# Performance work log

Measured on AMD Instinct MI355X. Metric: run time of the kernel, lower is better.

The kernel has to match this reference:

```python
import jax, jax.numpy as jnp
import numpy as np
from jax.scipy.linalg import expm

D_DYN = 512
STATIC_DIM = 64
U_DIM = 32
N_OBS = 20 * 2 + 10  # num_prod*2 + num_inj
BATCH = 512
T_STEPS = 256


def setup_inputs() -> dict:
    key = jax.random.key(0)
    ks = jax.random.split(key, 9)
    d = D_DYN
    return {
        "z_dyn": jax.random.normal(ks[0], (BATCH, d), jnp.float32),
        "z_static": jax.random.normal(ks[1], (BATCH, STATIC_DIM), jnp.float32),
        "dt": jax.random.uniform(ks[2], (1, 1), jnp.float32),
        "U": jax.random.normal(ks[3], (T_STEPS, BATCH, U_DIM), jnp.float32),
        "A_skew_params": (jax.random.normal(ks[4], (d * (d - 1) // 2,), jnp.float32) * 0.01),
        "gamma_raw": jnp.ones((d,), jnp.float32) * 0.5,
        "B_ct": jax.random.normal(ks[5], (d, U_DIM), jnp.float32) * (1.0 / np.sqrt(U_DIM)),
        "C": jax.random.normal(ks[6], (N_OBS, d), jnp.float32) * (1.0 / np.sqrt(d)),
        "D": jax.random.normal(ks[7], (N_OBS, U_DIM), jnp.float32) * (1.0 / np.sqrt(U_DIM)),
    }


def reference(z_dyn, z_static, dt, U, A_skew_params, gamma_raw, B_ct, C, D):
    d = z_dyn.shape[1]
    # Build continuous-time generator: skew-symmetric part minus positive diagonal damping.
    iu = jnp.triu_indices(d, k=1)
    A_skew = jnp.zeros((d, d), A_skew_params.dtype).at[iu].set(A_skew_params)
    A_skew = A_skew - A_skew.T
    A_ct = A_skew - jnp.diag(jax.nn.softplus(gamma_raw))
    # Exact ZOH discretization: A_bar = expm(A*dt), B_bar = A^{-1}(A_bar - I) B
    dt_val = dt[0, 0]
    A_bar = expm(A_ct * dt_val)
    B_bar = jnp.linalg.solve(A_ct, (A_bar - jnp.eye(d, dtype=A_ct.dtype)) @ B_ct)
    A_bar_T, B_bar_T, C_T, D_T = A_bar.T, B_bar.T, C.T, D.T

    def step(z, ut):
        z = z @ A_bar_T + ut @ B_bar_T          # [B, d]
        y = z @ C_T + (ut * dt) @ D_T           # [B, n_obs]
        return z, (z, y)

    _, (Z, Y) = jax.lax.scan(step, z_dyn, U)    # Z: [T, B, d], Y: [T, B, n_obs]
    return Z, Y
```

## Files before the change

### kernel.cpp

```cpp
#include <hip/hip_runtime.h>
#include <stdint.h>


typedef __bf16 bf16x8 __attribute__((ext_vector_type(8)));
typedef float  f32x4  __attribute__((ext_vector_type(4)));

#define NE  576
#define NE3 1728

__device__ __forceinline__ unsigned short f2bf(float x){
  union { float f; unsigned int u; } v; v.f = x;
  unsigned int r = (v.u + 0x7fffu + ((v.u >> 16) & 1u)) >> 16;
  return (unsigned short)r;
}
__device__ __forceinline__ float bf2f(unsigned short h){
  union { float f; unsigned int u; } v; v.u = ((unsigned int)h) << 16;
  return v.f;
}

__device__ __forceinline__ void gll16(const void* g, void* l){
  __builtin_amdgcn_global_load_lds((__attribute__((address_space(1))) void*)g,
                                   (__attribute__((address_space(3))) void*)l,
                                   16, 0, 0);
}

__global__ __launch_bounds__(256) void k_build_M(
    const float* __restrict__ skew, const float* __restrict__ gamma,
    const float* __restrict__ dtp, const float* __restrict__ B_ct,
    float* __restrict__ Xf, unsigned short* __restrict__ XAp,
    unsigned short* __restrict__ XBt){
  int id = blockIdx.x * 256 + threadIdx.x;
  if (id >= NE * NE) return;
  int r = id / NE, c = id % NE;
  float sc = dtp[0] * 0.25f;
  float v = 0.f;
  if (r < 512 && c < 512) {
    if (r < c) {
      long k = 511L * r - (long)r * (r - 1) / 2 + (c - r - 1);
      v = skew[k];
    } else if (r > c) {
      long k = 511L * c - (long)c * (c - 1) / 2 + (r - c - 1);
      v = -skew[k];
    } else {
      float g = gamma[r];
      float sp = (g > 20.f) ? g : log1pf(expf(g));
      v = -sp;
    }
  } else if (r < 512 && c >= 512 && c < 544) {
    v = B_ct[r * 32 + (c - 512)];
  }
  v *= sc;
  Xf[id] = v;
  unsigned short hi = f2bf(v);
  unsigned short lo = f2bf(v - bf2f(hi));
  XAp[(long)r * NE3 + c]          = hi;
  XAp[(long)r * NE3 + NE + c]     = hi;
  XAp[(long)r * NE3 + 2 * NE + c] = lo;
  XBt[(long)c * NE3 + r]          = hi;
  XBt[(long)c * NE3 + NE + r]     = lo;
  XBt[(long)c * NE3 + 2 * NE + r] = hi;
}

__global__ __launch_bounds__(256) void k_expm_gemm(
    const unsigned short* __restrict__ Ap, const unsigned short* __restrict__ Bt,
    const float* __restrict__ Cadd, float* __restrict__ outF,
    unsigned short* __restrict__ outAp, unsigned short* __restrict__ outBt){
  __shared__ __align__(16) unsigned short As[2][32 * 192];
  __shared__ __align__(16) unsigned short Bs[2][32 * 192];
  int tid = threadIdx.x, wave = tid >> 6, lane = tid & 63;
  int wm = wave & 1, wn = wave >> 1;
  int m0 = blockIdx.y * 32, n0 = blockIdx.x * 32;
  int lr = lane & 15, kq = lane >> 4;
  f32x4 acc = {0.f, 0.f, 0.f, 0.f};
  auto stage = [&](int buf, int kt){
    #pragma unroll
    for (int i = 0; i < 3; i++) {
      int base = i * 256 + wave * 64;
      int cc = base + lane;
      int rr = cc / 24, sl = cc - rr * 24;
      int ss = (sl & 24) | ((sl & 7) ^ (rr & 7));
      gll16(Ap + (long)(m0 + rr) * NE3 + kt + ss * 8, &As[buf][base * 8]);
      gll16(Bt + (long)(n0 + rr) * NE3 + kt + ss * 8, &Bs[buf][base * 8]);
    }
  };
  stage(0, 0);
  int cur = 0;
  for (int kt = 0; kt < NE3; kt += 192) {
    if (kt + 192 < NE3) {
      stage(cur ^ 1, kt + 192);
      asm volatile("s_waitcnt vmcnt(6)" ::: "memory");
    } else {
      asm volatile("s_waitcnt vmcnt(0)" ::: "memory");
    }
    __builtin_amdgcn_s_barrier();
    __builtin_amdgcn_sched_barrier(0);
    #pragma unroll
    for (int hh = 0; hh < 6; hh++) {
      int eo = (hh * 32 + kq * 8) ^ ((lr & 7) << 3);
      bf16x8 af = *(const bf16x8*)&As[cur][(wm * 16 + lr) * 192 + eo];
      bf16x8 bf = *(const bf16x8*)&Bs[cur][(wn * 16 + lr) * 192 + eo];
      acc = __builtin_amdgcn_mfma_f32_16x16x32_bf16(af, bf, acc, 0, 0, 0);
    }
    __builtin_amdgcn_s_barrier();
    cur ^= 1;
  }
  int n = n0 + wn * 16 + lr;
  for (int i = 0; i < 4; i++) {
    int m = m0 + wm * 16 + kq * 4 + i;
    float v = acc[i];
    if (Cadd) v += Cadd[(long)m * NE + n];
    if (outF) outF[(long)m * NE + n] = v;
    unsigned short hi = f2bf(v);
    unsigned short lo = f2bf(v - bf2f(hi));
    if (outAp) {
      outAp[(long)m * NE3 + n]          = hi;
      outAp[(long)m * NE3 + NE + n]     = hi;
      outAp[(long)m * NE3 + 2 * NE + n] = lo;
    }
    if (outBt) {
      outBt[(long)n * NE3 + m]          = hi;
      outBt[(long)n * NE3 + NE + m]     = lo;
      outBt[(long)n * NE3 + 2 * NE + m] = hi;
    }
  }
}

__global__ __launch_bounds__(256) void k_poly(
    const float* __restrict__ Xf, const float* __restrict__ X2f,
    const float* __restrict__ X3f, float* __restrict__ B0,
    unsigned short* __restrict__ B1Ap){
  int id = blockIdx.x * 256 + threadIdx.x;
  if (id >= NE * NE) return;
  int r = id / NE, c = id % NE;
  float x = Xf[id], x2 = X2f[id], x3 = X3f[id];
  float ii = (r == c) ? 1.f : 0.f;
  float b0 = ii + x + x2 * 0.5f + x3 * (1.f / 6.f);
  float b1 = ii * (1.f / 24.f) + x * (1.f / 120.f) + x2 * (1.f / 720.f) + x3 * (1.f / 5040.f);
  B0[id] = b0;
  unsigned short hi = f2bf(b1), lo = f2bf(b1 - bf2f(hi));
  B1Ap[(long)r * NE3 + c]          = hi;
  B1Ap[(long)r * NE3 + NE + c]     = hi;
  B1Ap[(long)r * NE3 + 2 * NE + c] = lo;
}

__global__ __launch_bounds__(256) void k_extract(
    const float* __restrict__ F, const float* __restrict__ Cin,
    unsigned short* __restrict__ WbigT, unsigned short* __restrict__ PT1,
    unsigned short* __restrict__ BbarT, unsigned short* __restrict__ G0,
    unsigned short* __restrict__ CA0){
  long id = (long)blockIdx.x * 256 + threadIdx.x;
  if (id < 512 * 512) {
    int m = (int)(id >> 9), k = (int)(id & 511);
    WbigT[(long)m * 1024 + k] = f2bf(F[(long)m * NE + k]);
    PT1[id] = f2bf(F[(long)k * NE + m]);
  }
  if (id < 512 * 32) {
    int dd = (int)(id >> 5), u = (int)(id & 31);
    unsigned short h = f2bf(F[(long)dd * NE + 512 + u]);
    G0[id] = h;
    BbarT[(long)u * 512 + dd] = h;
  }
  if (id < 64 * 512) {
    CA0[id] = (id < 50 * 512) ? f2bf(Cin[id]) : (unsigned short)0;
  }
}

template<int BM, int BN, int WM, int WN>
__global__ __launch_bounds__(256) void k_btgemm(
    const unsigned short* __restrict__ A, int ldA, long sAz,
    const unsigned short* __restrict__ Bt, int ldB, long sBz,
    unsigned short* __restrict__ C, int ldC, long sCz, int K,
    unsigned short* __restrict__ outT, int ldT, long sTz){
  constexpr int FM = BM / (16 * WM), FN = BN / (16 * WN);
  constexpr int LA = BM / 32, LB = BN / 32;
  __shared__ __align__(16) unsigned short As[2][BM * 64];
  __shared__ __align__(16) unsigned short Bs[2][BN * 64];
  int tid = threadIdx.x, wave = tid >> 6, lane = tid & 63;
  int wm = wave % WM, wn = wave / WM;
  long z = blockIdx.z;
  const unsigned short* Ab = A + z * sAz;
  const unsigned short* Bb = Bt + z * sBz;
  int m0 = blockIdx.y * BM, n0 = blockIdx.x * BN;
  int lr = lane & 15, kq = lane >> 4;
  f32x4 acc[FM][FN];
  f32x4 z4 = {0.f, 0.f, 0.f, 0.f};
  for (int i = 0; i < FM; i++) for (int j = 0; j < FN; j++) acc[i][j] = z4;
  auto stage = [&](int buf, int kt){
    #pragma unroll
    for (int i = 0; i < LA; i++) {
      int base = i * 256 + wave * 64;
      int cc = base + lane; int rr = cc >> 3, sl = cc & 7;
      gll16(Ab + (long)(m0 + rr) * ldA + kt + ((sl ^ (rr & 7)) << 3), &As[buf][base * 8]);
    }
    #pragma unroll
    for (int i = 0; i < LB; i++) {
      int base = i * 256 + wave * 64;
      int cc = base + lane; int rr = cc >> 3, sl = cc & 7;
      gll16(Bb + (long)(n0 + rr) * ldB + kt + ((sl ^ (rr & 7)) << 3), &Bs[buf][base * 8]);
    }
  };
  stage(0, 0);
  int cur = 0;
  for (int kt = 0; kt < K; kt += 64) {
    if (kt + 64 < K) {
      stage(cur ^ 1, kt + 64);
      asm volatile("s_waitcnt vmcnt(%0)" :: "i"(LA + LB) : "memory");
    } else {
      asm volatile("s_waitcnt vmcnt(0)" ::: "memory");
    }
    __builtin_amdgcn_s_barrier();
    __builtin_amdgcn_sched_barrier(0);
    #pragma unroll
    for (int h = 0; h < 2; h++) {
      int eo = (h * 32 + kq * 8) ^ ((lr & 7) << 3);
      bf16x8 af[FM], bfr[FN];
      #pragma unroll
      for (int i = 0; i < FM; i++)
        af[i] = *(const bf16x8*)&As[cur][(wm * (16 * FM) + i * 16 + lr) * 64 + eo];
      #pragma unroll
      for (int j = 0; j < FN; j++)
        bfr[j] = *(const bf16x8*)&Bs[cur][(wn * (16 * FN) + j * 16 + lr) * 64 + eo];
      #pragma unroll
      for (int i = 0; i < FM; i++)
        #pragma unroll
        for (int j = 0; j < FN; j++)
          acc[i][j] = __builtin_amdgcn_mfma_f32_16x16x32_bf16(af[i], bfr[j], acc[i][j], 0, 0, 0);
    }
    __builtin_amdgcn_s_barrier();
    cur ^= 1;
  }
  unsigned short* Cb = C + z * sCz;
  unsigned short* Tb = outT ? outT + z * sTz : nullptr;
  for (int i = 0; i < FM; i++)
    for (int j = 0; j < FN; j++) {
      int n = n0 + wn * (16 * FN) + j * 16 + lr;
      for (int r = 0; r < 4; r++) {
        int m = m0 + wm * (16 * FM) + i * 16 + kq * 4 + r;
        unsigned short hv = f2bf(acc[i][j][r]);
        Cb[(long)m * ldC + n] = hv;
        if (Tb) Tb[(long)n * ldT + m] = hv;
      }
    }
}

__global__ __launch_bounds__(256) void k_assembleUW(
    const unsigned short* __restrict__ G, const unsigned short* __restrict__ CA,
    const unsigned short* __restrict__ CG, const float* __restrict__ Din,
    const float* __restrict__ dtp, unsigned short* __restrict__ WbigT){
  long id = (long)blockIdx.x * 256 + threadIdx.x;
  if (id < 4194304) {
    int n = (int)(id >> 9), kk2 = (int)(id & 511);
    int j = (n >> 9) + 1, dcol = n & 511;
    int i = (kk2 >> 5) + 1, uu = kk2 & 31;
    unsigned short v = 0;
    if (i <= j) v = G[(long)(j - i) * 16384 + dcol * 32 + uu];
    WbigT[(long)n * 1024 + 512 + kk2] = v;
  } else {
    int id2 = (int)(id - 4194304);
    int np = id2 >> 10, kp = id2 & 1023;
    int jm1 = np >> 6, o = np & 63;
    unsigned short v;
    if (kp < 512) {
      v = CA[(long)(jm1 + 1) * 32768 + o * 512 + kp];
    } else {
      int i = ((kp - 512) >> 5) + 1, u = kp & 31;
      float f = 0.f;
      if (i <= jm1 + 1) f = bf2f(CG[(long)(jm1 + 1 - i) * 2048 + o * 32 + u]);
      if (i == jm1 + 1 && o < 50) f += dtp[0] * Din[o * 32 + u];
      v = f2bf(f);
    }
    WbigT[(long)(8192 + np) * 1024 + kp] = v;
  }
}

__global__ __launch_bounds__(256) void k_packX(
    const float* __restrict__ zdyn, const float* __restrict__ U,
    unsigned short* __restrict__ Xbuf){
  long id = (long)blockIdx.x * 256 + threadIdx.x;
  long c = id >> 19;
  int rem = (int)(id & ((1 << 19) - 1));
  int b = rem >> 10, col = rem & 1023;
  if (col < 512) {
    if (c == 0) Xbuf[id] = f2bf(zdyn[(long)b * 512 + col]);
  } else {
    int kk2 = col - 512;
    int t = (int)(c * 16) + (kk2 >> 5), uu = kk2 & 31;
    Xbuf[id] = f2bf(U[((long)t * 512 + b) * 32 + uu]);
  }
}

__global__ __launch_bounds__(256) void k_scanround(
    const unsigned short* __restrict__ Sin, int ldS, long sS,
    const unsigned short* __restrict__ R, int ldR,
    unsigned short* __restrict__ Out, int ldO, long sO, int h){
  __shared__ __align__(16) unsigned short As[2][64 * 64];
  __shared__ __align__(16) unsigned short Bs[2][64 * 64];
  int tid = threadIdx.x, wave = tid >> 6, lane = tid & 63;
  int wm = wave & 1, wn = wave >> 1;
  int c = blockIdx.z;
  int m0 = blockIdx.y * 64, n0 = blockIdx.x * 64;
  int lr = lane & 15, kq = lane >> 4;
  f32x4 acc[2][2];
  f32x4 z4 = {0.f, 0.f, 0.f, 0.f};
  for (int i = 0; i < 2; i++) for (int j = 0; j < 2; j++) acc[i][j] = z4;
  if (c >= h) {
    const unsigned short* Ab = Sin + (long)(c - h) * sS;
    auto stage = [&](int buf, int kt){
      #pragma unroll
      for (int i = 0; i < 2; i++) {
        int base = i * 256 + wave * 64;
        int cc = base + lane; int rr = cc >> 3, sl = cc & 7;
        gll16(Ab + (long)(m0 + rr) * ldS + kt + ((sl ^ (rr & 7)) << 3), &As[buf][base * 8]);
      }
      #pragma unroll
      for (int i = 0; i < 2; i++) {
        int base = i * 256 + wave * 64;
        int cc = base + lane; int rr = cc >> 3, sl = cc & 7;
        gll16(R + (long)(n0 + rr) * ldR + kt + ((sl ^ (rr & 7)) << 3), &Bs[buf][base * 8]);
      }
    };
    stage(0, 0);
    int cur = 0;
    for (int kt = 0; kt < 512; kt += 64) {
      if (kt + 64 < 512) {
        stage(cur ^ 1, kt + 64);
        asm volatile("s_waitcnt vmcnt(4)" ::: "memory");
      } else {
        asm volatile("s_waitcnt vmcnt(0)" ::: "memory");
      }
      __builtin_amdgcn_s_barrier();
      __builtin_amdgcn_sched_barrier(0);
      #pragma unroll
      for (int h2 = 0; h2 < 2; h2++) {
        int eo = (h2 * 32 + kq * 8) ^ ((lr & 7) << 3);
        bf16x8 af[2], bfr[2];
        #pragma unroll
        for (int i = 0; i < 2; i++)
          af[i] = *(const bf16x8*)&As[cur][(wm * 32 + i * 16 + lr) * 64 + eo];
        #pragma unroll
        for (int j = 0; j < 2; j++)
          bfr[j] = *(const bf16x8*)&Bs[cur][(wn * 32 + j * 16 + lr) * 64 + eo];
        #pragma unroll
        for (int i = 0; i < 2; i++)
          #pragma unroll
          for (int j = 0; j < 2; j++)
            acc[i][j] = __builtin_amdgcn_mfma_f32_16x16x32_bf16(af[i], bfr[j], acc[i][j], 0, 0, 0);
      }
      __builtin_amdgcn_s_barrier();
      cur ^= 1;
    }
  }
  const unsigned short* inC = Sin + (long)c * sS;
  unsigned short* OB = Out + (long)c * sO;
  for (int j = 0; j < 2; j++) {
    int n = n0 + wn * 32 + j * 16 + lr;
    for (int i = 0; i < 2; i++)
      for (int r = 0; r < 4; r++) {
        int m = m0 + wm * 32 + i * 16 + kq * 4 + r;
        float v = acc[i][j][r] + bf2f(inC[(long)m * ldS + n]);
        OB[(long)m * ldO + n] = f2bf(v);
      }
  }
}

__global__ __launch_bounds__(256) void k_mmbig(
    const unsigned short* __restrict__ Xall, const unsigned short* __restrict__ W,
    float* __restrict__ Zout, float* __restrict__ Yout){
  __shared__ __align__(16) unsigned short As[2][128 * 64];
  __shared__ __align__(16) unsigned short Bs[2][128 * 64];
  int tid = threadIdx.x, wave = tid >> 6, lane = tid & 63;
  int wm = wave & 1, wn = wave >> 1;
  int c = blockIdx.z;
  const unsigned short* Xc = Xall + (long)c * 524288;
  int m0 = blockIdx.y * 128, n0 = blockIdx.x * 128;
  int lr = lane & 15, kq = lane >> 4;
  f32x4 acc[4][4];
  f32x4 z4 = {0.f, 0.f, 0.f, 0.f};
  for (int i = 0; i < 4; i++) for (int j = 0; j < 4; j++) acc[i][j] = z4;
  auto stage = [&](int buf, int kt){
    #pragma unroll
    for (int i = 0; i < 4; i++) {
      int base = i * 256 + wave * 64;
      int cc = base + lane; int rr = cc >> 3, sl = cc & 7;
      gll16(Xc + (long)(m0 + rr) * 1024 + kt + ((sl ^ (rr & 7)) << 3), &As[buf][base * 8]);
    }
    #pragma unroll
    for (int i = 0; i < 4; i++) {
      int base = i * 256 + wave * 64;
      int cc = base + lane; int rr = cc >> 3, sl = cc & 7;
      gll16(W + (long)(n0 + rr) * 1024 + kt + ((sl ^ (rr & 7)) << 3), &Bs[buf][base * 8]);
    }
  };
  stage(0, 0);
  int cur = 0;
  for (int kt = 0; kt < 1024; kt += 64) {
    if (kt + 64 < 1024) {
      stage(cur ^ 1, kt + 64);
      asm volatile("s_waitcnt vmcnt(8)" ::: "memory");
    } else {
      asm volatile("s_waitcnt vmcnt(0)" ::: "memory");
    }
    __builtin_amdgcn_s_barrier();
    __builtin_amdgcn_sched_barrier(0);
    #pragma unroll
    for (int h = 0; h < 2; h++) {
      int eo = (h * 32 + kq * 8) ^ ((lr & 7) << 3);
      bf16x8 af[4], bfr[4];
      #pragma unroll
      for (int i = 0; i < 4; i++)
        af[i] = *(const bf16x8*)&As[cur][(wm * 64 + i * 16 + lr) * 64 + eo];
      #pragma unroll
      for (int j = 0; j < 4; j++)
        bfr[j] = *(const bf16x8*)&Bs[cur][(wn * 64 + j * 16 + lr) * 64 + eo];
      #pragma unroll
      for (int i = 0; i < 4; i++)
        #pragma unroll
        for (int j = 0; j < 4; j++)
          acc[i][j] = __builtin_amdgcn_mfma_f32_16x16x32_bf16(af[i], bfr[j], acc[i][j], 0, 0, 0);
    }
    __builtin_amdgcn_s_barrier();
    cur ^= 1;
  }
  int t0 = c * 16;
  if (n0 < 8192) {
    int jm1 = n0 >> 9;
    float* Zt = Zout + (long)(t0 + jm1) * 262144;
    for (int j = 0; j < 4; j++) {
      int n = n0 + wn * 64 + j * 16 + lr, dcol = n & 511;
      for (int i = 0; i < 4; i++)
        for (int r = 0; r < 4; r++) {
          int m = m0 + wm * 64 + i * 16 + kq * 4 + r;
          Zt[(long)m * 512 + dcol] = acc[i][j][r];
        }
    }
  } else {
    for (int j = 0; j < 4; j++) {
      int n = n0 + wn * 64 + j * 16 + lr;
      int q = n - 8192, jm1 = q >> 6, o = q & 63;
      if (o >= 50) continue;
      int t = t0 + jm1;
      for (int i = 0; i < 4; i++)
        for (int r = 0; r < 4; r++) {
          int m = m0 + wm * 64 + i * 16 + kq * 4 + r;
          Yout[((long)t * 512 + m) * 50 + o] = acc[i][j][r];
        }
    }
  }
}

static constexpr long NE2F = 331776L * 4;
static constexpr long SPLT = 995328L * 2;
static constexpr long OFF_XF   = 0;
static constexpr long OFF_X2F  = OFF_XF   + NE2F;
static constexpr long OFF_X3F  = OFF_X2F  + NE2F;
static constexpr long OFF_B0F  = OFF_X3F  + NE2F;
static constexpr long OFF_XAP  = OFF_B0F  + NE2F;
static constexpr long OFF_XBT  = OFF_XAP  + SPLT;
static constexpr long OFF_X2AP = OFF_XBT  + SPLT;
static constexpr long OFF_X2BT = OFF_X2AP + SPLT;
static constexpr long OFF_X4BT = OFF_X2BT + SPLT;
static constexpr long OFF_B1AP = OFF_X4BT + SPLT;
static constexpr long OFF_EAP  = OFF_B1AP + SPLT;
static constexpr long OFF_EBT  = OFF_EAP  + SPLT;
static constexpr long OFF_FAP  = OFF_EBT  + SPLT;
static constexpr long OFF_FBT  = OFF_FAP  + SPLT;
static constexpr long OFF_FF   = OFF_FBT  + SPLT;
static constexpr long OFF_WBT  = 0;
static constexpr long OFF_PT   = 18874368;
static constexpr long OFF_BBT  = OFF_PT  + 16L * 262144 * 2;
static constexpr long OFF_G    = OFF_BBT + 32768;
static constexpr long OFF_CA   = OFF_G   + 16L * 16384 * 2;
static constexpr long OFF_CG   = OFF_CA  + 17L * 32768 * 2;
static constexpr long OFF_XB   = OFF_PT;

extern "C" void kernel_launch(void* const* d_in, const int* in_sizes, int n_in,
                              void* d_out, int out_size, void* d_ws, size_t ws_size,
                              hipStream_t stream){
  const float* z_dyn = (const float*)d_in[0];
  const float* dtp   = (const float*)d_in[2];
  const float* U     = (const float*)d_in[3];
  const float* skew  = (const float*)d_in[4];
  const float* gamma = (const float*)d_in[5];
  const float* B_ct  = (const float*)d_in[6];
  const float* Cin   = (const float*)d_in[7];
  const float* Din   = (const float*)d_in[8];
  float* Zout = (float*)d_out;
  float* Yout = Zout + 67108864L;

  char* ws = (char*)d_ws;
  float* Xf  = (float*)(ws + OFF_XF);
  float* X2f = (float*)(ws + OFF_X2F);
  float* X3f = (float*)(ws + OFF_X3F);
  float* B0f = (float*)(ws + OFF_B0F);
  float* Ff  = (float*)(ws + OFF_FF);
  unsigned short* XAp  = (unsigned short*)(ws + OFF_XAP);
  unsigned short* XBt  = (unsigned short*)(ws + OFF_XBT);
  unsigned short* X2Ap = (unsigned short*)(ws + OFF_X2AP);
  unsigned short* X2Bt = (unsigned short*)(ws + OFF_X2BT);
  unsigned short* X4Bt = (unsigned short*)(ws + OFF_X4BT);
  unsigned short* B1Ap = (unsigned short*)(ws + OFF_B1AP);
  unsigned short* EAp  = (unsigned short*)(ws + OFF_EAP);
  unsigned short* EBt  = (unsigned short*)(ws + OFF_EBT);
  unsigned short* FAp  = (unsigned short*)(ws + OFF_FAP);
  unsigned short* FBt  = (unsigned short*)(ws + OFF_FBT);
  unsigned short* WbigT = (unsigned short*)(ws + OFF_WBT);
  unsigned short* PT    = (unsigned short*)(ws + OFF_PT);
  unsigned short* BbarT = (unsigned short*)(ws + OFF_BBT);
  unsigned short* Gar   = (unsigned short*)(ws + OFF_G);
  unsigned short* CAb   = (unsigned short*)(ws + OFF_CA);
  unsigned short* CGb   = (unsigned short*)(ws + OFF_CG);
  unsigned short* Xb    = (unsigned short*)(ws + OFF_XB);

  unsigned short* Sb  = (unsigned short*)Yout;
  unsigned short* M2b = Sb  + 4194304;
  unsigned short* TM2 = M2b + 262144;
  unsigned short* M4b = TM2 + 262144;
  unsigned short* TM4 = M4b + 262144;
  unsigned short* M8b = TM4 + 262144;

  dim3 b256(256);
  dim3 gE(18, 18);
  const long WBLK = 524288;
  const long PBLK = 262144;
  unsigned short* Wlast = WbigT + 15L * WBLK;

  k_build_M<<<dim3(1296), b256, 0, stream>>>(skew, gamma, dtp, B_ct, Xf, XAp, XBt);
  k_expm_gemm<<<gE, b256, 0, stream>>>(XAp,  XBt,  nullptr, X2f, X2Ap, X2Bt);
  k_expm_gemm<<<gE, b256, 0, stream>>>(X2Ap, XBt,  nullptr, X3f, nullptr, nullptr);
  k_expm_gemm<<<gE, b256, 0, stream>>>(X2Ap, X2Bt, nullptr, nullptr, nullptr, X4Bt);
  k_poly<<<dim3(1296), b256, 0, stream>>>(Xf, X2f, X3f, B0f, B1Ap);
  k_expm_gemm<<<gE, b256, 0, stream>>>(B1Ap, X4Bt, B0f, nullptr, EAp, EBt);
  k_expm_gemm<<<gE, b256, 0, stream>>>(EAp, EBt, nullptr, nullptr, FAp, FBt);
  k_expm_gemm<<<gE, b256, 0, stream>>>(FAp, FBt, nullptr, Ff, nullptr, nullptr);

  k_extract<<<dim3(1024), b256, 0, stream>>>(Ff, Cin, WbigT, PT, BbarT, Gar, CAb);

  k_btgemm<64,64,2,2><<<dim3(8,8,1), b256, 0, stream>>>(WbigT, 1024, 0, PT, 512, 0, WbigT + WBLK, 1024, 0, 512, PT + PBLK, 512, 0);
  k_btgemm<64,64,2,2><<<dim3(8,8,2), b256, 0, stream>>>(WbigT + WBLK, 1024, 0, PT, 512, PBLK, WbigT + 2*WBLK, 1024, WBLK, 512, PT + 2*PBLK, 512, PBLK);
  k_btgemm<64,64,2,2><<<dim3(8,8,4), b256, 0, stream>>>(WbigT + 3*WBLK, 1024, 0, PT, 512, PBLK, WbigT + 4*WBLK, 1024, WBLK, 512, PT + 4*PBLK, 512, PBLK);
  k_btgemm<64,64,2,2><<<dim3(8,8,8), b256, 0, stream>>>(WbigT + 7*WBLK, 1024, 0, PT, 512, PBLK, WbigT + 8*WBLK, 1024, WBLK, 512, PT + 8*PBLK, 512, PBLK);

  k_btgemm<64,64,2,2><<<dim3(8,8,1), b256, 0, stream>>>(Wlast, 1024, 0, PT + 15*PBLK, 512, 0, M2b, 512, 0, 512, TM2, 512, 0);
  k_btgemm<64,64,2,2><<<dim3(8,8,1), b256, 0, stream>>>(M2b, 512, 0, TM2, 512, 0, M4b, 512, 0, 512, TM4, 512, 0);
  k_btgemm<64,64,2,2><<<dim3(8,8,1), b256, 0, stream>>>(M4b, 512, 0, TM4, 512, 0, M8b, 512, 0, 512, nullptr, 0, 0);

  k_btgemm<64,32,4,1><<<dim3(1,8,15), b256, 0, stream>>>(WbigT, 1024, WBLK, BbarT, 512, 0, Gar + 16384, 32, 16384, 512, nullptr, 0, 0);
  k_btgemm<64,64,2,2><<<dim3(8,1,8), b256, 0, stream>>>(CAb, 512, 0, PT, 512, PBLK, CAb + 32768, 512, 32768, 512, nullptr, 0, 0);
  k_btgemm<64,64,2,2><<<dim3(8,1,8), b256, 0, stream>>>(CAb + 32768, 512, 32768, PT + 7*PBLK, 512, 0, CAb + 9L*32768, 512, 32768, 512, nullptr, 0, 0);
  k_btgemm<64,32,4,1><<<dim3(1,1,16), b256, 0, stream>>>(CAb, 512, 32768, BbarT, 512, 0, CGb, 32, 2048, 512, nullptr, 0, 0);

  k_assembleUW<<<dim3(20480), b256, 0, stream>>>(Gar, CAb, CGb, Din, dtp, WbigT);
  k_packX<<<dim3(32768), b256, 0, stream>>>(z_dyn, U, Xb);

  k_btgemm<64,64,2,2><<<dim3(8,8,15), b256, 0, stream>>>(
      Xb + 512, 1024, WBLK, Wlast + 512, 1024, 0,
      Xb + WBLK, 1024, WBLK, 512, nullptr, 0, 0);

  k_scanround<<<dim3(8,8,16), b256, 0, stream>>>(Xb, 1024, WBLK, Wlast, 1024, Sb, 512, PBLK, 1);
  k_scanround<<<dim3(8,8,16), b256, 0, stream>>>(Sb, 512, PBLK, M2b, 512, Xb, 1024, WBLK, 2);
  k_scanround<<<dim3(8,8,16), b256, 0, stream>>>(Xb, 1024, WBLK, M4b, 512, Sb, 512, PBLK, 4);
  k_scanround<<<dim3(8,8,16), b256, 0, stream>>>(Sb, 512, PBLK, M8b, 512, Xb, 1024, WBLK, 8);

  k_mmbig<<<dim3(72, 4, 16), b256, 0, stream>>>(Xb, WbigT, Zout, Yout);
}
```

Measured before the change: 683.2 us.

## Coalesce transposes via LDS, vectorize pack kernels, widen final GEMM to 512 threads

k_build_M and k_extract now run their transposed writes through a padded 32x33 shared-memory tile, so the transposed stores are coalesced instead of strided. k_assembleUW and k_packX each handle four elements per thread with vector loads and stores, and k_packX no longer launches idle threads for the z columns of later chunks. The final k_mmbig GEMM moves to 512 threads per block, each wave holding a 64x32 accumulator tile, with an adjusted vmcnt wait. The goal is to cut memory-transaction overhead in the setup kernels and raise occupancy in the big GEMM; the larger blocks could change register pressure and scheduling.

```diff
diff --git a/kernel.cpp b/kernel.cpp
--- a/kernel.cpp
+++ b/kernel.cpp
@@ -29,36 +29,52 @@
     const float* __restrict__ dtp, const float* __restrict__ B_ct,
     float* __restrict__ Xf, unsigned short* __restrict__ XAp,
     unsigned short* __restrict__ XBt){
-  int id = blockIdx.x * 256 + threadIdx.x;
-  if (id >= NE * NE) return;
-  int r = id / NE, c = id % NE;
+  __shared__ float T[32][33];
+  int bx = blockIdx.x % 18, by = blockIdx.x / 18;
+  int r0 = by * 32, c0 = bx * 32;
+  int tr = threadIdx.x >> 5, tc = threadIdx.x & 31;
   float sc = dtp[0] * 0.25f;
-  float v = 0.f;
-  if (r < 512 && c < 512) {
-    if (r < c) {
-      long k = 511L * r - (long)r * (r - 1) / 2 + (c - r - 1);
-      v = skew[k];
-    } else if (r > c) {
-      long k = 511L * c - (long)c * (c - 1) / 2 + (r - c - 1);
-      v = -skew[k];
-    } else {
-      float g = gamma[r];
-      float sp = (g > 20.f) ? g : log1pf(expf(g));
-      v = -sp;
-    }
-  } else if (r < 512 && c >= 512 && c < 544) {
-    v = B_ct[r * 32 + (c - 512)];
-  }
-  v *= sc;
-  Xf[id] = v;
-  unsigned short hi = f2bf(v);
-  unsigned short lo = f2bf(v - bf2f(hi));
-  XAp[(long)r * NE3 + c]          = hi;
-  XAp[(long)r * NE3 + NE + c]     = hi;
-  XAp[(long)r * NE3 + 2 * NE + c] = lo;
-  XBt[(long)c * NE3 + r]          = hi;
-  XBt[(long)c * NE3 + NE + r]     = lo;
-  XBt[(long)c * NE3 + 2 * NE + r] = hi;
+  #pragma unroll
+  for (int p = 0; p < 4; p++) {
+    int r = r0 + p * 8 + tr, c = c0 + tc;
+    float v = 0.f;
+    if (r < 512 && c < 512) {
+      if (r < c) {
+        long k = 511L * r - (long)r * (r - 1) / 2 + (c - r - 1);
+        v = skew[k];
+      } else if (r > c) {
+        long k = 511L * c - (long)c * (c - 1) / 2 + (r - c - 1);
+        v = -skew[k];
+      } else {
+        float g = gamma[r];
+        float sp = (g > 20.f) ? g : log1pf(expf(g));
+        v = -sp;
+      }
+    } else if (r < 512 && c >= 512 && c < 544) {
+      v = B_ct[r * 32 + (c - 512)];
+    }
+    v *= sc;
+    long id = (long)r * NE + c;
+    Xf[id] = v;
+    unsigned short hi = f2bf(v);
+    unsigned short lo = f2bf(v - bf2f(hi));
+    XAp[(long)r * NE3 + c]          = hi;
+    XAp[(long)r * NE3 + NE + c]     = hi;
+    XAp[(long)r * NE3 + 2 * NE + c] = lo;
+    T[p * 8 + tr][tc] = v;
+  }
+  __syncthreads();
+  #pragma unroll
+  for (int p = 0; p < 4; p++) {
+    int cl = p * 8 + tr, rl = tc;
+    float v = T[rl][cl];
+    unsigned short hi = f2bf(v);
+    unsigned short lo = f2bf(v - bf2f(hi));
+    long base = (long)(c0 + cl) * NE3 + r0;
+    XBt[base + rl]          = hi;
+    XBt[base + NE + rl]     = lo;
+    XBt[base + 2 * NE + rl] = hi;
+  }
 }
 
 __global__ __launch_bounds__(256) void k_expm_gemm(
@@ -148,20 +164,36 @@
     unsigned short* __restrict__ WbigT, unsigned short* __restrict__ PT1,
     unsigned short* __restrict__ BbarT, unsigned short* __restrict__ G0,
     unsigned short* __restrict__ CA0){
-  long id = (long)blockIdx.x * 256 + threadIdx.x;
-  if (id < 512 * 512) {
-    int m = (int)(id >> 9), k = (int)(id & 511);
-    WbigT[(long)m * 1024 + k] = f2bf(F[(long)m * NE + k]);
-    PT1[id] = f2bf(F[(long)k * NE + m]);
-  }
-  if (id < 512 * 32) {
-    int dd = (int)(id >> 5), u = (int)(id & 31);
-    unsigned short h = f2bf(F[(long)dd * NE + 512 + u]);
-    G0[id] = h;
-    BbarT[(long)u * 512 + dd] = h;
-  }
-  if (id < 64 * 512) {
-    CA0[id] = (id < 50 * 512) ? f2bf(Cin[id]) : (unsigned short)0;
+  int b = blockIdx.x;
+  if (b < 256) {
+    __shared__ float T[32][33];
+    int by = b >> 4, bx = b & 15;
+    int m0 = by * 32, k0 = bx * 32;
+    int tr = threadIdx.x >> 5, tc = threadIdx.x & 31;
+    #pragma unroll
+    for (int p = 0; p < 4; p++) {
+      int m = m0 + p * 8 + tr, k = k0 + tc;
+      float v = F[(long)m * NE + k];
+      WbigT[(long)m * 1024 + k] = f2bf(v);
+      T[p * 8 + tr][tc] = v;
+    }
+    __syncthreads();
+    #pragma unroll
+    for (int p = 0; p < 4; p++) {
+      int kl = p * 8 + tr, ml = tc;
+      PT1[(long)(k0 + kl) * 512 + m0 + ml] = f2bf(T[ml][kl]);
+    }
+  } else {
+    int id0 = (b - 256) * 256 + threadIdx.x;
+    for (int id = id0; id < 64 * 512; id += 1024) {
+      if (id < 512 * 32) {
+        int dd = id >> 5, u = id & 31;
+        unsigned short h = f2bf(F[(long)dd * NE + 512 + u]);
+        G0[id] = h;
+        BbarT[(long)u * 512 + dd] = h;
+      }
+      CA0[id] = (id < 50 * 512) ? f2bf(Cin[id]) : (unsigned short)0;
+    }
   }
 }
 
@@ -247,45 +279,59 @@
     const unsigned short* __restrict__ G, const unsigned short* __restrict__ CA,
     const unsigned short* __restrict__ CG, const float* __restrict__ Din,
     const float* __restrict__ dtp, unsigned short* __restrict__ WbigT){
-  long id = (long)blockIdx.x * 256 + threadIdx.x;
-  if (id < 4194304) {
-    int n = (int)(id >> 9), kk2 = (int)(id & 511);
+  long e = ((long)blockIdx.x * 256 + threadIdx.x) << 2;
+  if (e < 4194304) {
+    int n = (int)(e >> 9), kk2 = (int)(e & 511);
     int j = (n >> 9) + 1, dcol = n & 511;
     int i = (kk2 >> 5) + 1, uu = kk2 & 31;
-    unsigned short v = 0;
-    if (i <= j) v = G[(long)(j - i) * 16384 + dcol * 32 + uu];
-    WbigT[(long)n * 1024 + 512 + kk2] = v;
+    ushort4 h = {0, 0, 0, 0};
+    if (i <= j) h = *(const ushort4*)&G[(long)(j - i) * 16384 + dcol * 32 + uu];
+    *(ushort4*)&WbigT[(long)n * 1024 + 512 + kk2] = h;
   } else {
-    int id2 = (int)(id - 4194304);
+    int id2 = (int)(e - 4194304);
     int np = id2 >> 10, kp = id2 & 1023;
     int jm1 = np >> 6, o = np & 63;
-    unsigned short v;
+    ushort4 h;
     if (kp < 512) {
-      v = CA[(long)(jm1 + 1) * 32768 + o * 512 + kp];
+      h = *(const ushort4*)&CA[(long)(jm1 + 1) * 32768 + o * 512 + kp];
     } else {
       int i = ((kp - 512) >> 5) + 1, u = kp & 31;
-      float f = 0.f;
-      if (i <= jm1 + 1) f = bf2f(CG[(long)(jm1 + 1 - i) * 2048 + o * 32 + u]);
-      if (i == jm1 + 1 && o < 50) f += dtp[0] * Din[o * 32 + u];
-      v = f2bf(f);
-    }
-    WbigT[(long)(8192 + np) * 1024 + kp] = v;
+      float f0 = 0.f, f1 = 0.f, f2 = 0.f, f3 = 0.f;
+      if (i <= jm1 + 1) {
+        ushort4 g = *(const ushort4*)&CG[(long)(jm1 + 1 - i) * 2048 + o * 32 + u];
+        f0 = bf2f(g.x); f1 = bf2f(g.y); f2 = bf2f(g.z); f3 = bf2f(g.w);
+      }
+      if (i == jm1 + 1 && o < 50) {
+        float s = dtp[0];
+        f0 += s * Din[o * 32 + u];     f1 += s * Din[o * 32 + u + 1];
+        f2 += s * Din[o * 32 + u + 2]; f3 += s * Din[o * 32 + u + 3];
+      }
+      h.x = f2bf(f0); h.y = f2bf(f1); h.z = f2bf(f2); h.w = f2bf(f3);
+    }
+    *(ushort4*)&WbigT[(long)(8192 + np) * 1024 + kp] = h;
   }
 }
 
 __global__ __launch_bounds__(256) void k_packX(
     const float* __restrict__ zdyn, const float* __restrict__ U,
     unsigned short* __restrict__ Xbuf){
-  long id = (long)blockIdx.x * 256 + threadIdx.x;
-  long c = id >> 19;
-  int rem = (int)(id & ((1 << 19) - 1));
-  int b = rem >> 10, col = rem & 1023;
-  if (col < 512) {
-    if (c == 0) Xbuf[id] = f2bf(zdyn[(long)b * 512 + col]);
+  long id4 = (long)blockIdx.x * 256 + threadIdx.x;
+  if (id4 < 1048576) {
+    long e = id4 << 2;
+    long c = e >> 18; int rem = (int)(e & 262143);
+    int bb = rem >> 9, kk2 = rem & 511;
+    int t = (int)(c * 16) + (kk2 >> 5), uu = kk2 & 31;
+    float4 v = *(const float4*)&U[((long)t * 512 + bb) * 32 + uu];
+    ushort4 h; h.x = f2bf(v.x); h.y = f2bf(v.y); h.z = f2bf(v.z); h.w = f2bf(v.w);
+    *(ushort4*)&Xbuf[c * 524288 + (long)bb * 1024 + 512 + kk2] = h;
   } else {
-    int kk2 = col - 512;
-    int t = (int)(c * 16) + (kk2 >> 5), uu = kk2 & 31;
-    Xbuf[id] = f2bf(U[((long)t * 512 + b) * 32 + uu]);
+    long e = (id4 - 1048576) << 2;
+    if (e < 262144) {
+      int bb = (int)(e >> 9), col = (int)(e & 511);
+      float4 v = *(const float4*)&zdyn[(long)bb * 512 + col];
+      ushort4 h; h.x = f2bf(v.x); h.y = f2bf(v.y); h.z = f2bf(v.z); h.w = f2bf(v.w);
+      *(ushort4*)&Xbuf[(long)bb * 1024 + col] = h;
+    }
   }
 }
 
@@ -363,7 +409,7 @@
   }
 }
 
-__global__ __launch_bounds__(256) void k_mmbig(
+__global__ __launch_bounds__(512, 4) void k_mmbig(
     const unsigned short* __restrict__ Xall, const unsigned short* __restrict__ W,
     float* __restrict__ Zout, float* __restrict__ Yout){
   __shared__ __align__(16) unsigned short As[2][128 * 64];
@@ -374,21 +420,21 @@
   const unsigned short* Xc = Xall + (long)c * 524288;
   int m0 = blockIdx.y * 128, n0 = blockIdx.x * 128;
   int lr = lane & 15, kq = lane >> 4;
-  f32x4 acc[4][4];
+  f32x4 acc[4][2];
   f32x4 z4 = {0.f, 0.f, 0.f, 0.f};
-  for (int i = 0; i < 4; i++) for (int j = 0; j < 4; j++) acc[i][j] = z4;
+  for (int i = 0; i < 4; i++) for (int j = 0; j < 2; j++) acc[i][j] = z4;
   auto stage = [&](int buf, int kt){
     #pragma unroll
-    for (int i = 0; i < 4; i++) {
-      int base = i * 256 + wave * 64;
-      int cc = base + lane; int rr = cc >> 3, sl = cc & 7;
-      gll16(Xc + (long)(m0 + rr) * 1024 + kt + ((sl ^ (rr & 7)) << 3), &As[buf][base * 8]);
-    }
-    #pragma unroll
-    for (int i = 0; i < 4; i++) {
-      int base = i * 256 + wave * 64;
-      int cc = base + lane; int rr = cc >> 3, sl = cc & 7;
-      gll16(W + (long)(n0 + rr) * 1024 + kt + ((sl ^ (rr & 7)) << 3), &Bs[buf][base * 8]);
+    for (int i = 0; i < 2; i++) {
+      int cc = i * 512 + tid;
+      int rr = cc >> 3, sl = cc & 7;
+      gll16(Xc + (long)(m0 + rr) * 1024 + kt + ((sl ^ (rr & 7)) << 3), &As[buf][cc * 8]);
+    }
+    #pragma unroll
+    for (int i = 0; i < 2; i++) {
+      int cc = i * 512 + tid;
+      int rr = cc >> 3, sl = cc & 7;
+      gll16(W + (long)(n0 + rr) * 1024 + kt + ((sl ^ (rr & 7)) << 3), &Bs[buf][cc * 8]);
     }
   };
   stage(0, 0);
@@ -396,7 +442,7 @@
   for (int kt = 0; kt < 1024; kt += 64) {
     if (kt + 64 < 1024) {
       stage(cur ^ 1, kt + 64);
-      asm volatile("s_waitcnt vmcnt(8)" ::: "memory");
+      asm volatile("s_waitcnt vmcnt(4)" ::: "memory");
     } else {
       asm volatile("s_waitcnt vmcnt(0)" ::: "memory");
     }
@@ -405,17 +451,17 @@
     #pragma unroll
     for (int h = 0; h < 2; h++) {
       int eo = (h * 32 + kq * 8) ^ ((lr & 7) << 3);
-      bf16x8 af[4], bfr[4];
+      bf16x8 af[4], bfr[2];
       #pragma unroll
       for (int i = 0; i < 4; i++)
         af[i] = *(const bf16x8*)&As[cur][(wm * 64 + i * 16 + lr) * 64 + eo];
       #pragma unroll
-      for (int j = 0; j < 4; j++)
-        bfr[j] = *(const bf16x8*)&Bs[cur][(wn * 64 + j * 16 + lr) * 64 + eo];
+      for (int j = 0; j < 2; j++)
+        bfr[j] = *(const bf16x8*)&Bs[cur][(wn * 32 + j * 16 + lr) * 64 + eo];
       #pragma unroll
       for (int i = 0; i < 4; i++)
         #pragma unroll
-        for (int j = 0; j < 4; j++)
+        for (int j = 0; j < 2; j++)
           acc[i][j] = __builtin_amdgcn_mfma_f32_16x16x32_bf16(af[i], bfr[j], acc[i][j], 0, 0, 0);
     }
     __builtin_amdgcn_s_barrier();
@@ -425,8 +471,8 @@
   if (n0 < 8192) {
     int jm1 = n0 >> 9;
     float* Zt = Zout + (long)(t0 + jm1) * 262144;
-    for (int j = 0; j < 4; j++) {
-      int n = n0 + wn * 64 + j * 16 + lr, dcol = n & 511;
+    for (int j = 0; j < 2; j++) {
+      int n = n0 + wn * 32 + j * 16 + lr, dcol = n & 511;
       for (int i = 0; i < 4; i++)
         for (int r = 0; r < 4; r++) {
           int m = m0 + wm * 64 + i * 16 + kq * 4 + r;
@@ -434,8 +480,8 @@
         }
     }
   } else {
-    for (int j = 0; j < 4; j++) {
-      int n = n0 + wn * 64 + j * 16 + lr;
+    for (int j = 0; j < 2; j++) {
+      int n = n0 + wn * 32 + j * 16 + lr;
       int q = n - 8192, jm1 = q >> 6, o = q & 63;
       if (o >= 50) continue;
       int t = t0 + jm1;
@@ -524,7 +570,7 @@
   const long PBLK = 262144;
   unsigned short* Wlast = WbigT + 15L * WBLK;
 
-  k_build_M<<<dim3(1296), b256, 0, stream>>>(skew, gamma, dtp, B_ct, Xf, XAp, XBt);
+  k_build_M<<<dim3(324), b256, 0, stream>>>(skew, gamma, dtp, B_ct, Xf, XAp, XBt);
   k_expm_gemm<<<gE, b256, 0, stream>>>(XAp,  XBt,  nullptr, X2f, X2Ap, X2Bt);
   k_expm_gemm<<<gE, b256, 0, stream>>>(X2Ap, XBt,  nullptr, X3f, nullptr, nullptr);
   k_expm_gemm<<<gE, b256, 0, stream>>>(X2Ap, X2Bt, nullptr, nullptr, nullptr, X4Bt);
@@ -533,7 +579,7 @@
   k_expm_gemm<<<gE, b256, 0, stream>>>(EAp, EBt, nullptr, nullptr, FAp, FBt);
   k_expm_gemm<<<gE, b256, 0, stream>>>(FAp, FBt, nullptr, Ff, nullptr, nullptr);
 
-  k_extract<<<dim3(1024), b256, 0, stream>>>(Ff, Cin, WbigT, PT, BbarT, Gar, CAb);
+  k_extract<<<dim3(260), b256, 0, stream>>>(Ff, Cin, WbigT, PT, BbarT, Gar, CAb);
 
   k_btgemm<64,64,2,2><<<dim3(8,8,1), b256, 0, stream>>>(WbigT, 1024, 0, PT, 512, 0, WbigT + WBLK, 1024, 0, 512, PT + PBLK, 512, 0);
   k_btgemm<64,64,2,2><<<dim3(8,8,2), b256, 0, stream>>>(WbigT + WBLK, 1024, 0, PT, 512, PBLK, WbigT + 2*WBLK, 1024, WBLK, 512, PT + 2*PBLK, 512, PBLK);
@@ -549,8 +595,8 @@
   k_btgemm<64,64,2,2><<<dim3(8,1,8), b256, 0, stream>>>(CAb + 32768, 512, 32768, PT + 7*PBLK, 512, 0, CAb + 9L*32768, 512, 32768, 512, nullptr, 0, 0);
   k_btgemm<64,32,4,1><<<dim3(1,1,16), b256, 0, stream>>>(CAb, 512, 32768, BbarT, 512, 0, CGb, 32, 2048, 512, nullptr, 0, 0);
 
-  k_assembleUW<<<dim3(20480), b256, 0, stream>>>(Gar, CAb, CGb, Din, dtp, WbigT);
-  k_packX<<<dim3(32768), b256, 0, stream>>>(z_dyn, U, Xb);
+  k_assembleUW<<<dim3(5120), b256, 0, stream>>>(Gar, CAb, CGb, Din, dtp, WbigT);
+  k_packX<<<dim3(4353), b256, 0, stream>>>(z_dyn, U, Xb);
 
   k_btgemm<64,64,2,2><<<dim3(8,8,15), b256, 0, stream>>>(
       Xb + 512, 1024, WBLK, Wlast + 512, 1024, 0,
@@ -561,5 +607,5 @@
   k_scanround<<<dim3(8,8,16), b256, 0, stream>>>(Xb, 1024, WBLK, M4b, 512, Sb, 512, PBLK, 4);
   k_scanround<<<dim3(8,8,16), b256, 0, stream>>>(Sb, 512, PBLK, M8b, 512, Xb, 1024, WBLK, 8);
 
-  k_mmbig<<<dim3(72, 4, 16), b256, 0, stream>>>(Xb, WbigT, Zout, Yout);
-}
+  k_mmbig<<<dim3(72, 4, 16), dim3(512), 0, stream>>>(Xb, WbigT, Zout, Yout);
+}
```

New measurement: 695.9 us. About the same (+1.9%).
